# Kernel tuning notes

Measured on AMD Instinct MI355X. Metric: run time of the kernel, lower is better.

Reference implementation:

```python
import jax, jax.numpy as jnp
import numpy as np


def setup_inputs() -> dict:
    key = jax.random.key(0)
    ks = jax.random.split(key, 7)
    Bsz, Dm, L, N = 2, 1536, 2048, 16
    x = jax.random.normal(ks[0], (Bsz, Dm, L), jnp.float32)
    delta = jax.random.uniform(ks[1], (Bsz, Dm, L), jnp.float32, 1e-3, 0.1)  # positive step sizes
    A = -jax.random.uniform(ks[2], (Dm, N), jnp.float32, 0.5, 1.5)  # negative real A for stability
    B = jax.random.normal(ks[3], (Bsz, N, L), jnp.float32)
    C = jax.random.normal(ks[4], (Bsz, N, L), jnp.float32)
    D = jax.random.normal(ks[5], (Dm,), jnp.float32)
    z = jax.random.normal(ks[6], (Bsz, Dm, L), jnp.float32)
    return {"x": x, "delta": delta, "A": A, "B": B, "C": C, "D": D, "z": z}


def reference(x, delta, A, B, C, D, z):
    # x, delta, z: [b, d, l]; A: [d, n]; B, C: [b, n, l]; D: [d]
    dtype_in = x.dtype
    x = x.astype(jnp.float32)
    delta = delta.astype(jnp.float32)
    Bm = B.astype(jnp.float32)
    Cm = C.astype(jnp.float32)

    # time-major for scan: [l, b, ...]
    dl = jnp.moveaxis(delta, 2, 0)   # l b d
    xl = jnp.moveaxis(x, 2, 0)       # l b d
    Bl = jnp.moveaxis(Bm, 2, 0)      # l b n
    Cl = jnp.moveaxis(Cm, 2, 0)      # l b n

    h0 = jnp.zeros((x.shape[0], A.shape[0], A.shape[1]), jnp.float32)  # b d n

    def step(h, inp):
        d_t, x_t, B_t, C_t = inp
        deltaA = jnp.exp(d_t[:, :, None] * A[None, :, :])      # exp(einsum('bdl,dn->bdln')) at token t
        deltaB = d_t[:, :, None] * B_t[:, None, :]              # einsum('bdl,bnl->bdln') at token t
        h = deltaA * h + deltaB * x_t[:, :, None]               # Hx update
        y = jnp.einsum('bdn,bn->bd', h, C_t)                    # Yh readout
        return h, y

    _, ys = jax.lax.scan(step, h0, (dl, xl, Bl, Cl))            # ys: [l, b, d]
    y = jnp.moveaxis(ys, 0, 2)                                  # b d l

    out = y + x * D[None, :, None]
    out = out * jax.nn.silu(z)
    return out.astype(dtype_in)
```

## Files before the change

kernel.cpp:

```cpp
#include <hip/hip_runtime.h>
#include <hip/hip_fp16.h>

#define LOG2E 1.44269504088896340736f
#define DM 1536
#define LL  2048
#define NN  16
#define NCH 64
#define CL  32

__device__ __forceinline__ float fexp2(float v){ return __builtin_amdgcn_exp2f(v); }
__device__ __forceinline__ float frcp(float v){ return __builtin_amdgcn_rcpf(v); }

__device__ __forceinline__ float packdx(float d, float x){
    unsigned u = (unsigned)__half_as_ushort(__float2half_rn(d))
               | ((unsigned)__half_as_ushort(__float2half_rn(x)) << 16);
    return __uint_as_float(u);
}
__device__ __forceinline__ void unpackdx(float f, float& d, float& x){
    const unsigned u = __float_as_uint(f);
    d = __half2float(__ushort_as_half((unsigned short)(u & 0xffffu)));
    x = __half2float(__ushort_as_half((unsigned short)(u >> 16)));
}
__device__ __forceinline__ void unpack8(const float4 f, float* o){
    const unsigned u0=__float_as_uint(f.x), u1=__float_as_uint(f.y),
                   u2=__float_as_uint(f.z), u3=__float_as_uint(f.w);
    o[0]=__half2float(__ushort_as_half((unsigned short)(u0&0xffffu)));
    o[1]=__half2float(__ushort_as_half((unsigned short)(u0>>16)));
    o[2]=__half2float(__ushort_as_half((unsigned short)(u1&0xffffu)));
    o[3]=__half2float(__ushort_as_half((unsigned short)(u1>>16)));
    o[4]=__half2float(__ushort_as_half((unsigned short)(u2&0xffffu)));
    o[5]=__half2float(__ushort_as_half((unsigned short)(u2>>16)));
    o[6]=__half2float(__ushort_as_half((unsigned short)(u3&0xffffu)));
    o[7]=__half2float(__ushort_as_half((unsigned short)(u3>>16)));
}

__global__ __launch_bounds__(256) void transpose_bc(
        const float* __restrict__ Bm, const float* __restrict__ Cm,
        __half* __restrict__ BC){
    const int q  = blockIdx.x*256 + threadIdx.x;
    const int t0 = (q & 511) << 2;
    const int n  = (q >> 9) & 15;
    const int b  = q >> 13;
    const long i = (long)(b*NN + n)*LL + t0;
    const float4 bv = *(const float4*)(Bm + i);
    const float4 cv = *(const float4*)(Cm + i);
    const float bb[4]={bv.x,bv.y,bv.z,bv.w}, cc[4]={cv.x,cv.y,cv.z,cv.w};
#pragma unroll
    for (int j=0;j<4;++j){
        const int t = t0 + j;
        const long o = ((long)((b*CL + (t&31))*NCH + (t>>5)))*32 + n;
        BC[o]      = __float2half_rn(bb[j]);
        BC[o + 16] = __float2half_rn(cc[j]);
    }
}

__global__ __launch_bounds__(128, 2) void ssm_scan(
    const float* __restrict__ x, const float* __restrict__ delta,
    const float* __restrict__ A, const float* __restrict__ Dv,
    const float* __restrict__ z, const __half* __restrict__ BC,
    float* __restrict__ out)
{
    __shared__ float2 sdx[2][CL*64];

    const int lane = threadIdx.x & 63;
    const int w    = threadIdx.x >> 6;
    const int row0 = blockIdx.x*4 + w*2;
    const int b    = (row0 >= DM) ? 1 : 0;
    const int d0   = row0 - b*DM;
    float2* sw = sdx[w];

    const long base0 = (long)row0*LL;
    const long base1 = base0 + LL;
    const float* gd0 = delta + base0; const float* gx0 = x + base0;
    const float* gd1 = delta + base1; const float* gx1 = x + base1;

    for (int k=0;k<LL;k+=256){
        const int t0 = k + lane*4;
        const float4 dv0 = *(const float4*)(gd0 + t0);
        const float4 xv0 = *(const float4*)(gx0 + t0);
        const float4 dv1 = *(const float4*)(gd1 + t0);
        const float4 xv1 = *(const float4*)(gx1 + t0);
        const float dd0[4]={dv0.x,dv0.y,dv0.z,dv0.w}, xx0[4]={xv0.x,xv0.y,xv0.z,xv0.w};
        const float dd1[4]={dv1.x,dv1.y,dv1.z,dv1.w}, xx1[4]={xv1.x,xv1.y,xv1.z,xv1.w};
#pragma unroll
        for (int j=0;j<4;++j){
            const int t = t0 + j, r = t & 31, c = t >> 5;
            float2 wd; wd.x = packdx(dd0[j], xx0[j]); wd.y = packdx(dd1[j], xx1[j]);
            sw[r*64 + (c^r)] = wd;
        }
    }

    float A20[NN], A21[NN];
#pragma unroll
    for (int n=0;n<NN;++n){
        A20[n] = A[d0*NN+n]     * LOG2E;
        A21[n] = A[(d0+1)*NN+n] * LOG2E;
    }

    const __half* bc = BC + (long)b*65536 + lane*32;

    float G0[NN], G1[NN];
#pragma unroll
    for (int n=0;n<NN;++n){ G0[n]=0.f; G1[n]=0.f; }
    float ds0=0.f, ds1=0.f;
#pragma unroll 2
    for (int r=0;r<CL;++r){
        const float2 wd = sw[r*64 + (lane^r)];
        const float4* rec = (const float4*)(bc + (long)r*2048);
        float bb[16];
        unpack8(rec[0], bb); unpack8(rec[1], bb+8);
        float d_0,x_0,d_1,x_1;
        unpackdx(wd.x, d_0, x_0); unpackdx(wd.y, d_1, x_1);
        ds0 += d_0; ds1 += d_1;
        const float dx0 = d_0*x_0, dx1 = d_1*x_1;
#pragma unroll
        for (int n=0;n<NN;++n){
            const float e0 = fexp2(d_0*A20[n]);
            G0[n] = __builtin_fmaf(e0, G0[n], bb[n]*dx0);
            const float e1 = fexp2(d_1*A21[n]);
            G1[n] = __builtin_fmaf(e1, G1[n], bb[n]*dx1);
        }
    }

    float h0[NN], h1[NN];
    {
        float P0[NN], P1[NN];
#pragma unroll
        for (int n=0;n<NN;++n){ P0[n]=fexp2(ds0*A20[n]); P1[n]=fexp2(ds1*A21[n]); }
#pragma unroll
        for (int s=1;s<64;s<<=1){
#pragma unroll
            for (int n=0;n<NN;++n){
                const float pl0=__shfl_up(P0[n],s), gl0=__shfl_up(G0[n],s);
                const float pl1=__shfl_up(P1[n],s), gl1=__shfl_up(G1[n],s);
                if (lane >= s){
                    G0[n]=__builtin_fmaf(P0[n],gl0,G0[n]); P0[n]*=pl0;
                    G1[n]=__builtin_fmaf(P1[n],gl1,G1[n]); P1[n]*=pl1;
                }
            }
        }
#pragma unroll
        for (int n=0;n<NN;++n){
            const float g0=__shfl_up(G0[n],1), g1=__shfl_up(G1[n],1);
            h0[n] = (lane==0)?0.f:g0;
            h1[n] = (lane==0)?0.f:g1;
        }
    }

    const float Dd0 = Dv[d0], Dd1 = Dv[d0+1];
#pragma unroll 2
    for (int r=0;r<CL;++r){
        const int slot = r*64 + (lane^r);
        const float2 wd = sw[slot];
        const float4* rec = (const float4*)(bc + (long)r*2048);
        float bb[16], cc[16];
        unpack8(rec[0], bb); unpack8(rec[1], bb+8);
        unpack8(rec[2], cc); unpack8(rec[3], cc+8);
        float d_0,x_0,d_1,x_1;
        unpackdx(wd.x, d_0, x_0); unpackdx(wd.y, d_1, x_1);
        const float dx0 = d_0*x_0, dx1 = d_1*x_1;
        float ya0=0.f, yb0=0.f, ya1=0.f, yb1=0.f;
#pragma unroll
        for (int n=0;n<NN;n+=2){
            const float e0a = fexp2(d_0*A20[n]);
            h0[n]  =__builtin_fmaf(e0a,h0[n],  bb[n]*dx0);   ya0=__builtin_fmaf(h0[n],  cc[n],  ya0);
            const float e0b = fexp2(d_0*A20[n+1]);
            h0[n+1]=__builtin_fmaf(e0b,h0[n+1],bb[n+1]*dx0); yb0=__builtin_fmaf(h0[n+1],cc[n+1],yb0);
            const float e1a = fexp2(d_1*A21[n]);
            h1[n]  =__builtin_fmaf(e1a,h1[n],  bb[n]*dx1);   ya1=__builtin_fmaf(h1[n],  cc[n],  ya1);
            const float e1b = fexp2(d_1*A21[n+1]);
            h1[n+1]=__builtin_fmaf(e1b,h1[n+1],bb[n+1]*dx1); yb1=__builtin_fmaf(h1[n+1],cc[n+1],yb1);
        }
        float2 yo;
        yo.x = __builtin_fmaf(x_0, Dd0, ya0+yb0);
        yo.y = __builtin_fmaf(x_1, Dd1, ya1+yb1);
        sw[slot] = yo;
    }

    const float* gz0 = z + base0; const float* gz1 = z + base1;
    float* go0 = out + base0;     float* go1 = out + base1;
    for (int k=0;k<LL;k+=256){
        const int t0 = k + lane*4;
        const float4 zv0 = *(const float4*)(gz0 + t0);
        const float4 zv1 = *(const float4*)(gz1 + t0);
        const float zz0[4]={zv0.x,zv0.y,zv0.z,zv0.w}, zz1[4]={zv1.x,zv1.y,zv1.z,zv1.w};
        float o0[4], o1[4];
#pragma unroll
        for (int j=0;j<4;++j){
            const int t = t0 + j, r = t & 31, c = t >> 5;
            const float2 wd = sw[r*64 + (c^r)];
            const float s0 = frcp(1.f + fexp2(-zz0[j]*LOG2E));
            const float s1 = frcp(1.f + fexp2(-zz1[j]*LOG2E));
            o0[j] = wd.x * (zz0[j]*s0);
            o1[j] = wd.y * (zz1[j]*s1);
        }
        float4 a = {o0[0],o0[1],o0[2],o0[3]};
        float4 bq = {o1[0],o1[1],o1[2],o1[3]};
        *(float4*)(go0 + t0) = a;
        *(float4*)(go1 + t0) = bq;
    }
}

extern "C" void kernel_launch(void* const* d_in, const int* in_sizes, int n_in,
                              void* d_out, int out_size, void* d_ws, size_t ws_size,
                              hipStream_t stream) {
    const float* x     = (const float*)d_in[0];
    const float* delta = (const float*)d_in[1];
    const float* A     = (const float*)d_in[2];
    const float* B     = (const float*)d_in[3];
    const float* C     = (const float*)d_in[4];
    const float* Dv    = (const float*)d_in[5];
    const float* z     = (const float*)d_in[6];
    float* out = (float*)d_out;

    __half* BC = (__half*)d_ws;

    transpose_bc<<<dim3(64), dim3(256), 0, stream>>>(B, C, BC);
    ssm_scan<<<dim3((2*DM)/4), dim3(128), 0, stream>>>(x, delta, A, Dv, z, BC, out);
}
```

Measured before the change: 167.0 us.

## Split each row pair's sequence across two wavefronts with cross-wave carry

Each block now handles one pair of rows, and its two wavefronts split the sequence into 128 chunks of 16 steps instead of 64 chunks of 32. Wave 0's total prefix (P,G) passes through shared memory to wave 1 after a block barrier. This halves the serial per-lane chunk length and doubles the block count. Launch bounds are raised to three blocks per CU to fit more waves. The cost is an extra __syncthreads, a combine step and more chunk-level scan overhead.

```diff
diff --git a/kernel.cpp b/kernel.cpp
--- a/kernel.cpp
+++ b/kernel.cpp
@@ -5,8 +5,8 @@
 #define DM 1536
 #define LL  2048
 #define NN  16
-#define NCH 64
-#define CL  32
+#define NCH 128
+#define CL  16
 
 __device__ __forceinline__ float fexp2(float v){ return __builtin_amdgcn_exp2f(v); }
 __device__ __forceinline__ float frcp(float v){ return __builtin_amdgcn_rcpf(v); }
@@ -48,34 +48,35 @@
 #pragma unroll
     for (int j=0;j<4;++j){
         const int t = t0 + j;
-        const long o = ((long)((b*CL + (t&31))*NCH + (t>>5)))*32 + n;
+        const long o = ((long)((b*CL + (t&15))*NCH + (t>>4)))*32 + n;
         BC[o]      = __float2half_rn(bb[j]);
         BC[o + 16] = __float2half_rn(cc[j]);
     }
 }
 
-__global__ __launch_bounds__(128, 2) void ssm_scan(
+__global__ __launch_bounds__(128, 3) void ssm_scan(
     const float* __restrict__ x, const float* __restrict__ delta,
     const float* __restrict__ A, const float* __restrict__ Dv,
     const float* __restrict__ z, const __half* __restrict__ BC,
     float* __restrict__ out)
 {
-    __shared__ float2 sdx[2][CL*64];
+    __shared__ float2 sdx[CL*NCH];
+    __shared__ float  wtot[2][2][NN];
 
     const int lane = threadIdx.x & 63;
     const int w    = threadIdx.x >> 6;
-    const int row0 = blockIdx.x*4 + w*2;
+    const int row0 = blockIdx.x*2;
     const int b    = (row0 >= DM) ? 1 : 0;
     const int d0   = row0 - b*DM;
-    float2* sw = sdx[w];
+    const int cmy  = w*64 + lane;
 
     const long base0 = (long)row0*LL;
     const long base1 = base0 + LL;
     const float* gd0 = delta + base0; const float* gx0 = x + base0;
     const float* gd1 = delta + base1; const float* gx1 = x + base1;
 
-    for (int k=0;k<LL;k+=256){
-        const int t0 = k + lane*4;
+    for (int k=0;k<1024;k+=256){
+        const int t0 = w*1024 + k + lane*4;
         const float4 dv0 = *(const float4*)(gd0 + t0);
         const float4 xv0 = *(const float4*)(gx0 + t0);
         const float4 dv1 = *(const float4*)(gd1 + t0);
@@ -84,9 +85,9 @@
         const float dd1[4]={dv1.x,dv1.y,dv1.z,dv1.w}, xx1[4]={xv1.x,xv1.y,xv1.z,xv1.w};
 #pragma unroll
         for (int j=0;j<4;++j){
-            const int t = t0 + j, r = t & 31, c = t >> 5;
+            const int t = t0 + j, r = t & 15, c = t >> 4;
             float2 wd; wd.x = packdx(dd0[j], xx0[j]); wd.y = packdx(dd1[j], xx1[j]);
-            sw[r*64 + (c^r)] = wd;
+            sdx[r*NCH + (c^r)] = wd;
         }
     }
 
@@ -97,7 +98,7 @@
         A21[n] = A[(d0+1)*NN+n] * LOG2E;
     }
 
-    const __half* bc = BC + (long)b*65536 + lane*32;
+    const __half* bc = BC + (long)b*65536 + cmy*32;
 
     float G0[NN], G1[NN];
 #pragma unroll
@@ -105,8 +106,8 @@
     float ds0=0.f, ds1=0.f;
 #pragma unroll 2
     for (int r=0;r<CL;++r){
-        const float2 wd = sw[r*64 + (lane^r)];
-        const float4* rec = (const float4*)(bc + (long)r*2048);
+        const float2 wd = sdx[r*NCH + (cmy^r)];
+        const float4* rec = (const float4*)(bc + (long)r*4096);
         float bb[16];
         unpack8(rec[0], bb); unpack8(rec[1], bb+8);
         float d_0,x_0,d_1,x_1;
@@ -139,20 +140,33 @@
                 }
             }
         }
+        if (w==0 && lane==63){
+#pragma unroll
+            for (int n=0;n<NN;++n){
+                wtot[0][0][n]=P0[n]; wtot[1][0][n]=G0[n];
+                wtot[0][1][n]=P1[n]; wtot[1][1][n]=G1[n];
+            }
+        }
+        __syncthreads();
 #pragma unroll
         for (int n=0;n<NN;++n){
-            const float g0=__shfl_up(G0[n],1), g1=__shfl_up(G1[n],1);
-            h0[n] = (lane==0)?0.f:g0;
-            h1[n] = (lane==0)?0.f:g1;
+            const float pe0=__shfl_up(P0[n],1), ge0=__shfl_up(G0[n],1);
+            const float pe1=__shfl_up(P1[n],1), ge1=__shfl_up(G1[n],1);
+            const float Px0 = (lane==0)?1.f:pe0, Gx0 = (lane==0)?0.f:ge0;
+            const float Px1 = (lane==0)?1.f:pe1, Gx1 = (lane==0)?0.f:ge1;
+            const float Gt0 = (w==0)?0.f:wtot[1][0][n];
+            const float Gt1 = (w==0)?0.f:wtot[1][1][n];
+            h0[n] = __builtin_fmaf(Px0, Gt0, Gx0);
+            h1[n] = __builtin_fmaf(Px1, Gt1, Gx1);
         }
     }
 
     const float Dd0 = Dv[d0], Dd1 = Dv[d0+1];
 #pragma unroll 2
     for (int r=0;r<CL;++r){
-        const int slot = r*64 + (lane^r);
-        const float2 wd = sw[slot];
-        const float4* rec = (const float4*)(bc + (long)r*2048);
+        const int slot = r*NCH + (cmy^r);
+        const float2 wd = sdx[slot];
+        const float4* rec = (const float4*)(bc + (long)r*4096);
         float bb[16], cc[16];
         unpack8(rec[0], bb); unpack8(rec[1], bb+8);
         unpack8(rec[2], cc); unpack8(rec[3], cc+8);
@@ -174,27 +188,27 @@
         float2 yo;
         yo.x = __builtin_fmaf(x_0, Dd0, ya0+yb0);
         yo.y = __builtin_fmaf(x_1, Dd1, ya1+yb1);
-        sw[slot] = yo;
+        sdx[slot] = yo;
     }
 
     const float* gz0 = z + base0; const float* gz1 = z + base1;
     float* go0 = out + base0;     float* go1 = out + base1;
-    for (int k=0;k<LL;k+=256){
-        const int t0 = k + lane*4;
+    for (int k=0;k<1024;k+=256){
+        const int t0 = w*1024 + k + lane*4;
         const float4 zv0 = *(const float4*)(gz0 + t0);
         const float4 zv1 = *(const float4*)(gz1 + t0);
         const float zz0[4]={zv0.x,zv0.y,zv0.z,zv0.w}, zz1[4]={zv1.x,zv1.y,zv1.z,zv1.w};
         float o0[4], o1[4];
 #pragma unroll
         for (int j=0;j<4;++j){
-            const int t = t0 + j, r = t & 31, c = t >> 5;
-            const float2 wd = sw[r*64 + (c^r)];
+            const int t = t0 + j, r = t & 15, c = t >> 4;
+            const float2 wd = sdx[r*NCH + (c^r)];
             const float s0 = frcp(1.f + fexp2(-zz0[j]*LOG2E));
             const float s1 = frcp(1.f + fexp2(-zz1[j]*LOG2E));
             o0[j] = wd.x * (zz0[j]*s0);
             o1[j] = wd.y * (zz1[j]*s1);
         }
-        float4 a = {o0[0],o0[1],o0[2],o0[3]};
+        float4 a  = {o0[0],o0[1],o0[2],o0[3]};
         float4 bq = {o1[0],o1[1],o1[2],o1[3]};
         *(float4*)(go0 + t0) = a;
         *(float4*)(go1 + t0) = bq;
@@ -216,5 +230,5 @@
     __half* BC = (__half*)d_ws;
 
     transpose_bc<<<dim3(64), dim3(256), 0, stream>>>(B, C, BC);
-    ssm_scan<<<dim3((2*DM)/4), dim3(128), 0, stream>>>(x, delta, A, Dv, z, BC, out);
-}
+    ssm_scan<<<dim3(DM), dim3(128), 0, stream>>>(x, delta, A, Dv, z, BC, out);
+}
```

Result: faster. 156.4 us (-6.4%).
